# Kernel optimization log

Hardware: AMD Instinct MI355X
Metric: run time of the kernel (lower is better)

The kernel has to match this reference:

```python
import jax, jax.numpy as jnp
import numpy as np

N = 50000        # nodes
E = 800000       # edges
F_IN = 128       # dataset.num_features (== dim*heads so all conv layers share in_channels)
DIM = 32         # mParams['dim']
HEADS = 4        # mParams['num_heads']
HC = DIM * HEADS # 128
DEPTH = 2        # mParams['c_depth'] -> total conv layers = DEPTH + 1 = 3
L = DEPTH + 1
DIM2 = 16        # ceil(DIM/2)
NCLS = 6
SLOPE = 0.2      # GATv2Conv default negative_slope


def setup_inputs() -> dict:
    key = jax.random.key(0)
    ks = jax.random.split(key, 20)
    def lin(k, fan_in, shape):
        return jax.random.normal(k, shape, dtype=jnp.float32) / np.sqrt(fan_in)
    x = jax.random.normal(ks[0], (N, F_IN), dtype=jnp.float32)
    edge_index = jax.random.randint(ks[1], (2, E), 0, N, dtype=jnp.int64)
    batch = jnp.zeros((N,), dtype=jnp.int64)
    # stacked GATv2Conv params (all layers have in_channels = 128)
    Wl = lin(ks[2], F_IN, (L, F_IN, HC))   # lin_l weight (source transform)
    Wr = lin(ks[3], F_IN, (L, F_IN, HC))   # lin_r weight (target transform)
    bl = jnp.zeros((L, HC), dtype=jnp.float32)
    br = jnp.zeros((L, HC), dtype=jnp.float32)
    att = lin(ks[4], DIM, (L, HEADS, DIM)) # attention vector a
    cb = jnp.zeros((L, HC), dtype=jnp.float32)  # conv output bias
    W1 = lin(ks[5], HC, (HC, DIM));   b1 = jnp.zeros((DIM,), jnp.float32)
    W2 = lin(ks[6], DIM, (DIM, DIM2)); b2 = jnp.zeros((DIM2,), jnp.float32)
    W3 = lin(ks[7], 2 * DIM2, (2 * DIM2, NCLS)); b3 = jnp.zeros((NCLS,), jnp.float32)
    return {"x": x, "edge_index": edge_index, "batch": batch,
            "Wl": Wl, "Wr": Wr, "bl": bl, "br": br, "att": att, "cb": cb,
            "W1": W1, "b1": b1, "W2": W2, "b2": b2, "W3": W3, "b3": b3}


def _gatv2_layer(h, src, dst, Wl, Wr, bl, br, att, cb):
    # h: [N, F]; src/dst: [Ea] (self-loops included)
    xl = (h @ Wl + bl).reshape(N, HEADS, DIM)  # source-side transform
    xr = (h @ Wr + br).reshape(N, HEADS, DIM)  # target-side transform
    msg = xl[src] + xr[dst]                    # [Ea, H, C]
    e = jnp.where(msg > 0, msg, SLOPE * msg)   # leaky_relu
    score = jnp.einsum('ehc,hc->eh', e, att)   # [Ea, H]
    # scatter-softmax over destination nodes
    m = jax.ops.segment_max(score, dst, num_segments=N)        # [N, H]
    ex = jnp.exp(score - m[dst])
    s = jax.ops.segment_sum(ex, dst, num_segments=N)           # [N, H]
    alpha = ex / (s[dst] + 1e-16)                              # [Ea, H]
    out = jax.ops.segment_sum(alpha[:, :, None] * xl[src], dst, num_segments=N)
    return out.reshape(N, HC) + cb


def reference(x, edge_index, batch, Wl, Wr, bl, br, att, cb, W1, b1, W2, b2, W3, b3):
    src0, dst0 = edge_index[0], edge_index[1]
    loop = jnp.arange(N, dtype=edge_index.dtype)
    src = jnp.concatenate([src0, loop])  # GATv2Conv add_self_loops=True
    dst = jnp.concatenate([dst0, loop])
    h = x
    for i in range(L):
        h = jax.nn.relu(_gatv2_layer(h, src, dst, Wl[i], Wr[i], bl[i], br[i], att[i], cb[i]))
    h = jax.nn.relu(h @ W1 + b1)
    h = jax.nn.relu(h @ W2 + b2)
    # dropout(p=0.5) is identity in eval mode
    e = jnp.concatenate([h[src0], h[dst0]], axis=1)  # [E, 2*DIM2]
    out = e @ W3 + b3                                # [E, NCLS]
    return (out, e)
```

## Files before the change

### kernel.cpp

```cpp
#include <hip/hip_runtime.h>
#include <hip/hip_bf16.h>

typedef __hip_bfloat16 bf16;
typedef __attribute__((ext_vector_type(8))) short bf16x8;
typedef __attribute__((ext_vector_type(4))) float f32x4;

#define N_NODES 50000
#define E_EDGES 800000
#define EA (E_EDGES + N_NODES)
#define HC 128
#define HEADS 4
#define DIM 32
#define DIM2 16
#define NCLS 6
#define SLOPE 0.2f
#define XN (N_NODES * HC)
#define GM 32
#define HSTRIDE 152
#define WSWZ_L 32768
#define NCHUNK ((N_NODES + 1023) / 1024)

#define P_CVTI (2 * E_EDGES)
#define P_PRM  6390
#define P_WSWZ (3 * WSWZ_L)
#define P_TOT  (P_CVTI + P_PRM + P_WSWZ)

__device__ __forceinline__ float b2f(bf16 v) { return __bfloat162float(v); }
__device__ __forceinline__ unsigned short f2bfu(float f) {
    bf16 b = __float2bfloat16(f);
    return *(unsigned short*)&b;
}
__device__ __forceinline__ unsigned packbf(float a, float b) {
    return (unsigned)f2bfu(a) | ((unsigned)f2bfu(b) << 16);
}

__device__ __forceinline__ void block_detect(const void* wptr, const void* eptr,
                                             int* det, int& isf32, int& is64) {
    int tid = threadIdx.x;
    if (tid == 0) { det[0] = 0; det[1] = 0; }
    __syncthreads();
    const unsigned short* w = (const unsigned short*)wptr;
    int badf = 0;
    for (int i = tid; i < 1024; i += 256) {
        unsigned v = w[i];
        unsigned ex = (v >> 7) & 0xFF;
        if (v != 0 && (ex < 90 || ex > 150)) badf++;
    }
    const int* ei = (const int*)eptr;
    int nz = 0;
    for (int i = tid; i < 1024; i += 256) {
        if (ei[2 * i + 1] != 0) nz++;
    }
    if (badf) atomicAdd(&det[0], badf);
    if (nz)   atomicAdd(&det[1], nz);
    __syncthreads();
    isf32 = det[0] > 100;
    is64  = det[1] < 100;
}

__global__ __launch_bounds__(256) void k_prep(
        const void* eraw, const void* sWl, const void* sWr,
        const void* sbl, const void* sbr, const void* satt, const void* scb,
        const void* sW1, const void* sb1, const void* sW2, const void* sb2,
        const void* sW3, const void* sb3,
        int* __restrict__ eidx, int* __restrict__ off,
        float* __restrict__ prm, unsigned short* __restrict__ wswz) {
    __shared__ int det[2];
    int isf32, is64;
    block_detect(sWl, eraw, det, isf32, is64);

    int i = blockIdx.x * 256 + threadIdx.x;
    if (i < P_CVTI) {
        int v = is64 ? (int)((const long long*)eraw)[i] : ((const int*)eraw)[i];
        if (v < 0) v = 0;
        if (v >= N_NODES) v = N_NODES - 1;
        eidx[i] = v;
        if (i >= E_EDGES) atomicAdd(&off[v], 1);
        return;
    }
    i -= P_CVTI;
    if (i < P_PRM) {
        int j = i + 98304;
        const void* src; float* dst; int o;
        if      (j < 98688)  { src = sbl;  dst = prm + 98304;  o = j - 98304; }
        else if (j < 99072)  { src = sbr;  dst = prm + 98688;  o = j - 98688; }
        else if (j < 99456)  { src = satt; dst = prm + 99072;  o = j - 99072; }
        else if (j < 99840)  { src = scb;  dst = prm + 99456;  o = j - 99456; }
        else if (j < 103936) { src = sW1;  dst = prm + 99840;  o = j - 99840; }
        else if (j < 103968) { src = sb1;  dst = prm + 103936; o = j - 103936; }
        else if (j < 104480) { src = sW2;  dst = prm + 103968; o = j - 103968; }
        else if (j < 104496) { src = sb2;  dst = prm + 104480; o = j - 104480; }
        else if (j < 104688) { src = sW3;  dst = prm + 104496; o = j - 104496; }
        else                 { src = sb3;  dst = prm + 104688; o = j - 104688; }
        dst[o] = isf32 ? ((const float*)src)[o] : b2f(((const bf16*)src)[o]);
        return;
    }
    i -= P_PRM;
    if (i >= P_WSWZ) return;
    int L = i / WSWZ_L;
    int e = i % WSWZ_L;
    int ntile = e >> 11;
    int r2 = e & 2047;
    int ks = r2 >> 9;
    int r3 = r2 & 511;
    int lane = r3 >> 3;
    int j = r3 & 7;
    int col = ntile * 16 + (lane & 15);
    int k = ks * 32 + (lane >> 4) * 8 + j;
    const void* src = (col < HC) ? sWl : sWr;
    int idx = L * HC * HC + k * HC + (col & (HC - 1));
    float v = isf32 ? ((const float*)src)[idx] : b2f(((const bf16*)src)[idx]);
    wswz[i] = f2bfu(v);
}

__global__ __launch_bounds__(1024) void k_scan1(int* __restrict__ off, int* __restrict__ part) {
    __shared__ int s[1024];
    int tid = threadIdx.x;
    int i = blockIdx.x * 1024 + tid;
    int v = (i < N_NODES) ? off[i] + 1 : 0;
    s[tid] = v;
    __syncthreads();
    for (int o = 1; o < 1024; o <<= 1) {
        int t = (tid >= o) ? s[tid - o] : 0;
        __syncthreads();
        s[tid] += t;
        __syncthreads();
    }
    if (i < N_NODES) off[i] = s[tid] - v;
    if (tid == 1023) part[blockIdx.x] = s[1023];
}

__global__ __launch_bounds__(64) void k_scan2(int* __restrict__ part) {
    int tid = threadIdx.x;
    int v = (tid < NCHUNK) ? part[tid] : 0;
    int orig = v;
    for (int o = 1; o < 64; o <<= 1) {
        int t = __shfl_up(v, o);
        if (tid >= o) v += t;
    }
    if (tid < NCHUNK) part[tid] = v - orig;
}

__global__ __launch_bounds__(1024) void k_scan3(int* __restrict__ off, const int* __restrict__ part) {
    int i = blockIdx.x * 1024 + threadIdx.x;
    if (i < N_NODES) off[i] += part[blockIdx.x];
    if (i == 0) off[N_NODES] = EA;
}

__global__ void k_scatter(const int* __restrict__ eidx, const int* __restrict__ off,
                          int* __restrict__ fill, int* __restrict__ csrsrc) {
    int e = blockIdx.x * blockDim.x + threadIdx.x;
    if (e >= EA) return;
    int src, dst;
    if (e < E_EDGES) { src = eidx[e]; dst = eidx[E_EDGES + e]; }
    else             { src = dst = e - E_EDGES; }
    int pos = off[dst] + atomicAdd(&fill[dst], 1);
    if (pos >= 0 && pos < EA) csrsrc[pos] = src;
}

__global__ __launch_bounds__(256) void k_gemm_mfma(
        const void* __restrict__ hsrc, const void* wdet, const void* edet,
        int detect_in,
        const unsigned short* __restrict__ wswz,
        const float* __restrict__ bl, const float* __restrict__ br,
        unsigned* __restrict__ xlbf, float* __restrict__ xr) {
    __shared__ unsigned short hs[GM * HSTRIDE];
    __shared__ int det[2];
    int tid = threadIdx.x;
    int wave = tid >> 6, lane = tid & 63;
    long row0 = (long)blockIdx.x * GM;

    int f32in = 0;
    if (detect_in) {
        int is64d;
        block_detect(wdet, edet, det, f32in, is64d);
    }

    if (f32in) {
        for (int idx = tid; idx < GM * 64; idx += 256) {
            int r = idx >> 6, cp = idx & 63;
            float v0 = 0.f, v1 = 0.f;
            if (row0 + r < N_NODES) {
                const float2 hv = ((const float2*)((const float*)hsrc + (row0 + r) * HC))[cp];
                v0 = hv.x; v1 = hv.y;
            }
            *(unsigned*)&hs[r * HSTRIDE + cp * 2] = packbf(v0, v1);
        }
    } else {
        for (int idx = tid; idx < GM * 64; idx += 256) {
            int r = idx >> 6, cp = idx & 63;
            unsigned u = 0;
            if (row0 + r < N_NODES)
                u = ((const unsigned*)hsrc)[(row0 + r) * (HC / 2) + cp];
            *(unsigned*)&hs[r * HSTRIDE + cp * 2] = u;
        }
    }
    __syncthreads();

    int q = lane >> 4, l16 = lane & 15;
    for (int nt = 0; nt < 4; nt++) {
        int colbase = wave * 64 + nt * 16;
        int col = colbase + l16;
        int ntile = colbase >> 4;
        f32x4 acc0 = {0.f, 0.f, 0.f, 0.f};
        f32x4 acc1 = {0.f, 0.f, 0.f, 0.f};
#pragma unroll
        for (int ks = 0; ks < 4; ks++) {
            bf16x8 bfrag = *(const bf16x8*)(wswz + (((ntile * 4 + ks) * 64 + lane) << 3));
            bf16x8 a0 = *(const bf16x8*)(hs + l16 * HSTRIDE + ks * 32 + q * 8);
            bf16x8 a1 = *(const bf16x8*)(hs + (16 + l16) * HSTRIDE + ks * 32 + q * 8);
            acc0 = __builtin_amdgcn_mfma_f32_16x16x32_bf16(a0, bfrag, acc0, 0, 0, 0);
            acc1 = __builtin_amdgcn_mfma_f32_16x16x32_bf16(a1, bfrag, acc1, 0, 0, 0);
        }
        if (col < HC) {
            float bias = bl[col];
#pragma unroll
            for (int reg = 0; reg < 4; reg++) {
                float v0 = acc0[reg] + bias;
                float v1 = acc1[reg] + bias;
                float p0 = __shfl_xor(v0, 1);
                float p1 = __shfl_xor(v1, 1);
                if ((lane & 1) == 0) {
                    long n0 = row0 + q * 4 + reg;
                    long n1 = row0 + 16 + q * 4 + reg;
                    unsigned u0 = packbf(v0, p0);
                    unsigned u1 = packbf(v1, p1);
                    int cp = col >> 1;
                    if (n0 < N_NODES) xlbf[n0 * (HC / 2) + cp] = u0;
                    if (n1 < N_NODES) xlbf[n1 * (HC / 2) + cp] = u1;
                }
            }
        } else {
            int c = col - HC;
            float bias = br[c];
#pragma unroll
            for (int reg = 0; reg < 4; reg++) {
                long n0 = row0 + q * 4 + reg;
                long n1 = row0 + 16 + q * 4 + reg;
                if (n0 < N_NODES) xr[n0 * HC + c] = acc0[reg] + bias;
                if (n1 < N_NODES) xr[n1 * HC + c] = acc1[reg] + bias;
            }
        }
    }
}

__global__ __launch_bounds__(256) void k_attn(
        const unsigned* __restrict__ xlbf, const float* __restrict__ xr,
        const int* __restrict__ off, const int* __restrict__ csrsrc,
        const float* __restrict__ att, const float* __restrict__ cb,
        void* __restrict__ hout, int out_bf16) {
    int wave = threadIdx.x >> 6;
    int lane = threadIdx.x & 63;
    int node = blockIdx.x * 4 + wave;
    if (node >= N_NODES) return;
    int grp = lane >> 4;
    int gl  = lane & 15;
    int fb  = gl * 8;
    int head = fb >> 5;

    const float4* xrp = (const float4*)(xr + (long)node * HC + fb);
    float4 xa = xrp[0], xb = xrp[1];
    const float4* ap = (const float4*)(att + head * DIM + (fb & 31));
    float4 aa = ap[0], ab = ap[1];

    int e0 = off[node], e1 = off[node + 1];
    if (e0 < 0) e0 = 0;
    if (e1 > EA) e1 = EA;
    if (e1 <= e0) {
        if (grp == 0) {
            if (out_bf16) {
                uint4 z = {0u, 0u, 0u, 0u};
                *(uint4*)((unsigned*)hout + (long)node * (HC / 2) + gl * 4) = z;
            } else {
                float4 z = make_float4(0.f, 0.f, 0.f, 0.f);
                ((float4*)((float*)hout + (long)node * HC + fb))[0] = z;
                ((float4*)((float*)hout + (long)node * HC + fb))[1] = z;
            }
        }
        return;
    }
    int klast = e1 - 1;

    int k0 = e0 + grp;
    int ka = k0 < klast ? k0 : klast;
    int kb = (k0 + 4) < klast ? (k0 + 4) : klast;
    int sa = csrsrc[ka];
    int sb = csrsrc[kb];
    uint4 u0 = ((const uint4*)(xlbf + (long)sa * (HC / 2)))[gl];
    uint4 u1 = ((const uint4*)(xlbf + (long)sb * (HC / 2)))[gl];

    float m = -1e30f, ssum = 0.f;
    float acc[8];
#pragma unroll
    for (int j = 0; j < 8; j++) acc[j] = 0.f;

    for (int kk = k0; kk < e1; kk += 4) {
        uint4 cur = u0;
        u0 = u1;
        int kp = (kk + 8) < klast ? (kk + 8) : klast;
        int sp = csrsrc[kp];
        u1 = ((const uint4*)(xlbf + (long)sp * (HC / 2)))[gl];

        float x0 = __uint_as_float(cur.x << 16);
        float x1 = __uint_as_float(cur.x & 0xffff0000u);
        float x2 = __uint_as_float(cur.y << 16);
        float x3 = __uint_as_float(cur.y & 0xffff0000u);
        float x4 = __uint_as_float(cur.z << 16);
        float x5 = __uint_as_float(cur.z & 0xffff0000u);
        float x6 = __uint_as_float(cur.w << 16);
        float x7 = __uint_as_float(cur.w & 0xffff0000u);
        float m0 = x0 + xa.x, m1 = x1 + xa.y, m2 = x2 + xa.z, m3 = x3 + xa.w;
        float m4 = x4 + xb.x, m5 = x5 + xb.y, m6 = x6 + xb.z, m7 = x7 + xb.w;
        float l0 = fmaxf(m0, SLOPE * m0), l1 = fmaxf(m1, SLOPE * m1);
        float l2 = fmaxf(m2, SLOPE * m2), l3 = fmaxf(m3, SLOPE * m3);
        float l4 = fmaxf(m4, SLOPE * m4), l5 = fmaxf(m5, SLOPE * m5);
        float l6 = fmaxf(m6, SLOPE * m6), l7 = fmaxf(m7, SLOPE * m7);
        float p = l0 * aa.x + l1 * aa.y + l2 * aa.z + l3 * aa.w
                + l4 * ab.x + l5 * ab.y + l6 * ab.z + l7 * ab.w;
        p += __shfl_xor(p, 1);
        p += __shfl_xor(p, 2);
        float mn = fmaxf(m, p);
        float sc = __expf(m - mn);
        float ex = __expf(p - mn);
        ssum = ssum * sc + ex;
        acc[0] = acc[0] * sc + ex * x0;
        acc[1] = acc[1] * sc + ex * x1;
        acc[2] = acc[2] * sc + ex * x2;
        acc[3] = acc[3] * sc + ex * x3;
        acc[4] = acc[4] * sc + ex * x4;
        acc[5] = acc[5] * sc + ex * x5;
        acc[6] = acc[6] * sc + ex * x6;
        acc[7] = acc[7] * sc + ex * x7;
        m = mn;
    }

#pragma unroll
    for (int d = 16; d <= 32; d <<= 1) {
        float mo = __shfl_xor(m, d);
        float so = __shfl_xor(ssum, d);
        float ao[8];
#pragma unroll
        for (int j = 0; j < 8; j++) ao[j] = __shfl_xor(acc[j], d);
        float mn = fmaxf(m, mo);
        float s1 = __expf(m - mn);
        float s2 = __expf(mo - mn);
        ssum = ssum * s1 + so * s2;
#pragma unroll
        for (int j = 0; j < 8; j++) acc[j] = acc[j] * s1 + ao[j] * s2;
        m = mn;
    }

    if (grp == 0) {
        float inv = 1.f / (ssum + 1e-16f);
        const float4* cbp = (const float4*)(cb + fb);
        float4 c0 = cbp[0], c1 = cbp[1];
        float o0 = fmaxf(acc[0] * inv + c0.x, 0.f);
        float o1 = fmaxf(acc[1] * inv + c0.y, 0.f);
        float o2 = fmaxf(acc[2] * inv + c0.z, 0.f);
        float o3 = fmaxf(acc[3] * inv + c0.w, 0.f);
        float o4 = fmaxf(acc[4] * inv + c1.x, 0.f);
        float o5 = fmaxf(acc[5] * inv + c1.y, 0.f);
        float o6 = fmaxf(acc[6] * inv + c1.z, 0.f);
        float o7 = fmaxf(acc[7] * inv + c1.w, 0.f);
        if (out_bf16) {
            uint4 w;
            w.x = packbf(o0, o1);
            w.y = packbf(o2, o3);
            w.z = packbf(o4, o5);
            w.w = packbf(o6, o7);
            *(uint4*)((unsigned*)hout + (long)node * (HC / 2) + gl * 4) = w;
        } else {
            float4 a0 = make_float4(o0, o1, o2, o3);
            float4 a1 = make_float4(o4, o5, o6, o7);
            float4* op = (float4*)((float*)hout + (long)node * HC + fb);
            op[0] = a0;
            op[1] = a1;
        }
    }
}

__global__ __launch_bounds__(256) void k_mlp(
        const float* __restrict__ h, const float* __restrict__ W1,
        const float* __restrict__ b1, const float* __restrict__ W2,
        const float* __restrict__ b2, float* __restrict__ h3) {
    __shared__ float w1s[HC * DIM];
    __shared__ float hs[16 * HC];
    __shared__ float h2s[16 * DIM];
    __shared__ float w2s[DIM * DIM2];
    int tid = threadIdx.x;
    long row0 = (long)blockIdx.x * 16;
    for (int idx = tid; idx < HC * DIM; idx += 256) w1s[idx] = W1[idx];
    for (int idx = tid; idx < DIM * DIM2; idx += 256) w2s[idx] = W2[idx];
    for (int idx = tid; idx < 16 * HC; idx += 256) {
        long g = row0 * HC + idx;
        hs[idx] = (g < (long)N_NODES * HC) ? h[g] : 0.f;
    }
    __syncthreads();
#pragma unroll
    for (int p = 0; p < 2; p++) {
        int idx = tid + p * 256;
        int r = idx >> 5, c = idx & 31;
        float acc = b1[c];
        for (int k = 0; k < HC; k++) acc += hs[r * HC + k] * w1s[k * DIM + c];
        h2s[r * DIM + c] = acc > 0.f ? acc : 0.f;
    }
    __syncthreads();
    int r = tid >> 4, c = tid & 15;
    float acc = b2[c];
    for (int k = 0; k < DIM; k++) acc += h2s[r * DIM + k] * w2s[k * DIM2 + c];
    long row = row0 + r;
    if (row < N_NODES) h3[row * DIM2 + c] = acc > 0.f ? acc : 0.f;
}

__global__ __launch_bounds__(256) void k_out(
        const float* __restrict__ h3, const int* __restrict__ eidx,
        const float* __restrict__ W3, const float* __restrict__ b3,
        void* __restrict__ dout, const void* wdet, const void* edet) {
    __shared__ float w3s[2 * DIM2 * NCLS];
    __shared__ float bs[NCLS];
    __shared__ int det[2];
    int isf32, is64d;
    block_detect(wdet, edet, det, isf32, is64d);
    int tid = threadIdx.x;
    if (tid < 2 * DIM2 * NCLS) w3s[tid] = W3[tid];
    if (tid < NCLS) bs[tid] = b3[tid];
    __syncthreads();
    int e = blockIdx.x * 256 + tid;
    if (e >= E_EDGES) return;
    int src = eidx[e], dst = eidx[E_EDGES + e];
    float v[2 * DIM2];
    const float4* ps = (const float4*)(h3 + (long)src * DIM2);
    const float4* pd = (const float4*)(h3 + (long)dst * DIM2);
#pragma unroll
    for (int q = 0; q < 4; q++) {
        float4 t = ps[q];
        v[q * 4 + 0] = t.x; v[q * 4 + 1] = t.y; v[q * 4 + 2] = t.z; v[q * 4 + 3] = t.w;
    }
#pragma unroll
    for (int q = 0; q < 4; q++) {
        float4 t = pd[q];
        v[16 + q * 4 + 0] = t.x; v[16 + q * 4 + 1] = t.y; v[16 + q * 4 + 2] = t.z; v[16 + q * 4 + 3] = t.w;
    }
    float o[NCLS];
#pragma unroll
    for (int j = 0; j < NCLS; j++) {
        float acc = bs[j];
#pragma unroll
        for (int k = 0; k < 2 * DIM2; k++) acc += v[k] * w3s[k * NCLS + j];
        o[j] = acc;
    }
    if (isf32) {
        float* out0 = (float*)dout;
#pragma unroll
        for (int j = 0; j < NCLS; j++) out0[(long)e * NCLS + j] = o[j];
        float4* eo = (float4*)((float*)dout + (long)E_EDGES * NCLS) + (long)e * 8;
#pragma unroll
        for (int q = 0; q < 8; q++)
            eo[q] = make_float4(v[q * 4], v[q * 4 + 1], v[q * 4 + 2], v[q * 4 + 3]);
    } else {
        bf16* out0 = (bf16*)dout;
#pragma unroll
        for (int j = 0; j < NCLS; j++) out0[(long)e * NCLS + j] = __float2bfloat16(o[j]);
        uint4* eo = (uint4*)((bf16*)dout + (long)E_EDGES * NCLS) + (long)e * 4;
#pragma unroll
        for (int q = 0; q < 4; q++) {
            uint4 w;
            w.x = packbf(v[q * 8 + 0], v[q * 8 + 1]);
            w.y = packbf(v[q * 8 + 2], v[q * 8 + 3]);
            w.z = packbf(v[q * 8 + 4], v[q * 8 + 5]);
            w.w = packbf(v[q * 8 + 6], v[q * 8 + 7]);
            eo[q] = w;
        }
    }
}

extern "C" void kernel_launch(void* const* d_in, const int* in_sizes, int n_in,
                              void* d_out, int out_size, void* d_ws, size_t ws_size,
                              hipStream_t stream) {
    float* wsf   = (float*)d_ws;
    float* h     = wsf + 16;
    float* xl    = h  + (long)N_NODES * HC;
    float* xr    = xl + (long)N_NODES * HC;
    float* prm   = xr + (long)N_NODES * HC;
    unsigned short* wswz = (unsigned short*)(prm + 110000);
    int*   eidx  = (int*)(wswz + P_WSWZ);
    int*   off   = eidx + 2 * E_EDGES;
    int*   fill  = off + (N_NODES + 1);
    int*   csr   = fill + N_NODES;
    int*   part  = csr + EA;
    unsigned* xlbf = (unsigned*)xl;
    float* h3 = xl;

    float* pbl = prm + 98304;
    float* pbr = prm + 98688;
    float* patt= prm + 99072;
    float* pcb = prm + 99456;
    float* pW1 = prm + 99840;
    float* pb1 = prm + 103936;
    float* pW2 = prm + 103968;
    float* pb2 = prm + 104480;
    float* pW3 = prm + 104496;
    float* pb3 = prm + 104688;

    hipMemsetAsync(off, 0, (size_t)(2 * N_NODES + 1) * sizeof(int), stream);

    k_prep<<<(P_TOT + 255) / 256, 256, 0, stream>>>(
        d_in[1], d_in[3], d_in[4], d_in[5], d_in[6], d_in[7], d_in[8],
        d_in[9], d_in[10], d_in[11], d_in[12], d_in[13], d_in[14],
        eidx, off, prm, wswz);

    k_scan1<<<NCHUNK, 1024, 0, stream>>>(off, part);
    k_scan2<<<1, 64, 0, stream>>>(part);
    k_scan3<<<NCHUNK, 1024, 0, stream>>>(off, part);
    k_scatter<<<(EA + 255) / 256, 256, 0, stream>>>(eidx, off, fill, csr);

    for (int i = 0; i < 3; i++) {
        k_gemm_mfma<<<(N_NODES + GM - 1) / GM, 256, 0, stream>>>(
            i == 0 ? (const void*)d_in[0] : (const void*)h,
            d_in[3], d_in[1], i == 0 ? 1 : 0,
            wswz + (long)i * WSWZ_L, pbl + (long)i * HC, pbr + (long)i * HC,
            xlbf, xr);
        k_attn<<<(N_NODES + 3) / 4, 256, 0, stream>>>(
            xlbf, xr, off, csr, patt + (long)i * HEADS * DIM, pcb + (long)i * HC,
            (void*)h, i < 2 ? 1 : 0);
    }

    k_mlp<<<(N_NODES + 15) / 16, 256, 0, stream>>>(h, pW1, pb1, pW2, pb2, h3);

    k_out<<<(E_EDGES + 255) / 256, 256, 0, stream>>>(h3, eidx, pW3, pb3, d_out,
                                                     d_in[3], d_in[1]);
}
```

Before: 574.8 us.

## Fuse scan kernels, deepen attention gather prefetch, vectorize output stores

Removes the separate k_scan2 launch: each k_scan3 block now sums the partial counts of the preceding chunks itself with a wavefront reduction. The attention loop now loads CSR source indices one step further ahead and computes gather addresses with 32-bit shifts, which should hide more of the index-load latency. The edge output kernel writes the six class logits as paired float2 or packed bf16 stores instead of scalar stores. Costs are one extra index prefetch register and redundant small reductions in each scan block.

```diff
diff --git a/kernel.cpp b/kernel.cpp
--- a/kernel.cpp
+++ b/kernel.cpp
@@ -130,20 +130,17 @@
     if (tid == 1023) part[blockIdx.x] = s[1023];
 }
 
-__global__ __launch_bounds__(64) void k_scan2(int* __restrict__ part) {
+__global__ __launch_bounds__(1024) void k_scan3(int* __restrict__ off, const int* __restrict__ part) {
+    __shared__ int sbase;
     int tid = threadIdx.x;
-    int v = (tid < NCHUNK) ? part[tid] : 0;
-    int orig = v;
-    for (int o = 1; o < 64; o <<= 1) {
-        int t = __shfl_up(v, o);
-        if (tid >= o) v += t;
-    }
-    if (tid < NCHUNK) part[tid] = v - orig;
-}
-
-__global__ __launch_bounds__(1024) void k_scan3(int* __restrict__ off, const int* __restrict__ part) {
-    int i = blockIdx.x * 1024 + threadIdx.x;
-    if (i < N_NODES) off[i] += part[blockIdx.x];
+    if (tid < 64) {
+        int v = (tid < NCHUNK && tid < (int)blockIdx.x) ? part[tid] : 0;
+        for (int o = 32; o > 0; o >>= 1) v += __shfl_down(v, o);
+        if (tid == 0) sbase = v;
+    }
+    __syncthreads();
+    int i = blockIdx.x * 1024 + tid;
+    if (i < N_NODES) off[i] += sbase;
     if (i == 0) off[N_NODES] = EA;
 }
 
@@ -280,14 +277,18 @@
         return;
     }
     int klast = e1 - 1;
+    const char* xlb = (const char*)xlbf;
+    unsigned glo = (unsigned)gl * 16u;
 
     int k0 = e0 + grp;
     int ka = k0 < klast ? k0 : klast;
     int kb = (k0 + 4) < klast ? (k0 + 4) : klast;
-    int sa = csrsrc[ka];
-    int sb = csrsrc[kb];
-    uint4 u0 = ((const uint4*)(xlbf + (long)sa * (HC / 2)))[gl];
-    uint4 u1 = ((const uint4*)(xlbf + (long)sb * (HC / 2)))[gl];
+    int kc = (k0 + 8) < klast ? (k0 + 8) : klast;
+    int s0 = csrsrc[ka];
+    int s1 = csrsrc[kb];
+    int s2 = csrsrc[kc];
+    uint4 u0 = *(const uint4*)(xlb + (((unsigned)s0 << 8) + glo));
+    uint4 u1 = *(const uint4*)(xlb + (((unsigned)s1 << 8) + glo));
 
     float m = -1e30f, ssum = 0.f;
     float acc[8];
@@ -297,9 +298,10 @@
     for (int kk = k0; kk < e1; kk += 4) {
         uint4 cur = u0;
         u0 = u1;
-        int kp = (kk + 8) < klast ? (kk + 8) : klast;
-        int sp = csrsrc[kp];
-        u1 = ((const uint4*)(xlbf + (long)sp * (HC / 2)))[gl];
+        int sg = s2;
+        int kn = (kk + 12) < klast ? (kk + 12) : klast;
+        s2 = csrsrc[kn];
+        u1 = *(const uint4*)(xlb + (((unsigned)sg << 8) + glo));
 
         float x0 = __uint_as_float(cur.x << 16);
         float x1 = __uint_as_float(cur.x & 0xffff0000u);
@@ -342,11 +344,11 @@
 #pragma unroll
         for (int j = 0; j < 8; j++) ao[j] = __shfl_xor(acc[j], d);
         float mn = fmaxf(m, mo);
-        float s1 = __expf(m - mn);
-        float s2 = __expf(mo - mn);
-        ssum = ssum * s1 + so * s2;
-#pragma unroll
-        for (int j = 0; j < 8; j++) acc[j] = acc[j] * s1 + ao[j] * s2;
+        float s1f = __expf(m - mn);
+        float s2f = __expf(mo - mn);
+        ssum = ssum * s1f + so * s2f;
+#pragma unroll
+        for (int j = 0; j < 8; j++) acc[j] = acc[j] * s1f + ao[j] * s2f;
         m = mn;
     }
 
@@ -450,17 +452,19 @@
         o[j] = acc;
     }
     if (isf32) {
-        float* out0 = (float*)dout;
-#pragma unroll
-        for (int j = 0; j < NCLS; j++) out0[(long)e * NCLS + j] = o[j];
+        float2* out0 = (float2*)dout;
+        out0[(long)e * 3 + 0] = make_float2(o[0], o[1]);
+        out0[(long)e * 3 + 1] = make_float2(o[2], o[3]);
+        out0[(long)e * 3 + 2] = make_float2(o[4], o[5]);
         float4* eo = (float4*)((float*)dout + (long)E_EDGES * NCLS) + (long)e * 8;
 #pragma unroll
         for (int q = 0; q < 8; q++)
             eo[q] = make_float4(v[q * 4], v[q * 4 + 1], v[q * 4 + 2], v[q * 4 + 3]);
     } else {
-        bf16* out0 = (bf16*)dout;
-#pragma unroll
-        for (int j = 0; j < NCLS; j++) out0[(long)e * NCLS + j] = __float2bfloat16(o[j]);
+        unsigned* out0 = (unsigned*)dout;
+        out0[(long)e * 3 + 0] = packbf(o[0], o[1]);
+        out0[(long)e * 3 + 1] = packbf(o[2], o[3]);
+        out0[(long)e * 3 + 2] = packbf(o[4], o[5]);
         uint4* eo = (uint4*)((bf16*)dout + (long)E_EDGES * NCLS) + (long)e * 4;
 #pragma unroll
         for (int q = 0; q < 4; q++) {
@@ -510,7 +514,6 @@
         eidx, off, prm, wswz);
 
     k_scan1<<<NCHUNK, 1024, 0, stream>>>(off, part);
-    k_scan2<<<1, 64, 0, stream>>>(part);
     k_scan3<<<NCHUNK, 1024, 0, stream>>>(off, part);
     k_scatter<<<(EA + 255) / 256, 256, 0, stream>>>(eidx, off, fill, csr);
 
```

Result: slower. 597.9 us (+4.0%).
